# Performance work log

Measured on AMD Instinct MI355X. Metric: run time of the kernel, lower is better.

The kernel has to match this reference:

```python
import jax, jax.numpy as jnp
import numpy as np

B, N, D = 8, 1024, 1024
H = 16
HD = D // H  # 64
SCALE = float(HD) ** -0.5


def setup_inputs() -> dict:
    key = jax.random.key(0)
    k1, k2, k3 = jax.random.split(key, 3)
    x = jax.random.normal(k1, (B, N, D), dtype=jnp.float32)
    W_qkv = jax.random.normal(k2, (D, 3 * D), dtype=jnp.float32) * (D ** -0.5)
    b_qkv = jnp.zeros((3 * D,), dtype=jnp.float32)
    W_o = jax.random.normal(k3, (D, D), dtype=jnp.float32) * (D ** -0.5)
    b_o = jnp.zeros((D,), dtype=jnp.float32)
    return {"x": x, "W_qkv": W_qkv, "b_qkv": b_qkv, "W_o": W_o, "b_o": b_o}


def reference(x, W_qkv, b_qkv, W_o, b_o):
    b, n, _ = x.shape
    qkv = x @ W_qkv + b_qkv                      # (B, N, 3D)
    qkv = qkv.reshape(b, n, H, 3 * HD).transpose(0, 2, 1, 3)  # (B, H, N, 3*HD)
    q, k, v = jnp.split(qkv, 3, axis=-1)          # each (B, H, N, HD)
    attn = jnp.einsum('bhnd,bhmd->bhnm', q, k) * SCALE
    attn = jax.nn.softmax(attn, axis=-1)          # (B, H, N, N); dropout p=0 -> identity
    heads = jnp.einsum('bhnm,bhmd->bhnd', attn, v)
    heads = heads.transpose(0, 2, 1, 3).reshape(b, n, H * HD)  # (B, N, D)
    return heads @ W_o + b_o
```

## Files before the change

### kernel.cpp

```cpp
#include <hip/hip_runtime.h>
#include <hip/hip_bf16.h>

typedef unsigned short ushort_t;
typedef __bf16 bf16x8 __attribute__((ext_vector_type(8)));
typedef float floatx4 __attribute__((ext_vector_type(4)));

#define MFMA(a, b, c) __builtin_amdgcn_mfma_f32_16x16x32_bf16(a, b, c, 0, 0, 0)

__device__ __forceinline__ float b2f(ushort_t u) {
    union { ushort_t u; __hip_bfloat16 h; } cvt; cvt.u = u; return __bfloat162float(cvt.h);
}
__device__ __forceinline__ ushort_t f2b(float f) {
    union { ushort_t u; __hip_bfloat16 h; } cvt; cvt.h = __float2bfloat16(f); return cvt.u;
}

__device__ __forceinline__ void async_copy16(const ushort_t* g, ushort_t* l) {
    __builtin_amdgcn_global_load_lds(
        (const __attribute__((address_space(1))) void*)g,
        (__attribute__((address_space(3))) void*)l, 16, 0, 0);
}

__global__ void convert_x(const float* __restrict__ xin, ushort_t* __restrict__ xb) {
    int i = blockIdx.x * 256 + threadIdx.x;
    const float4* xf = (const float4*)xin;
    float4 a = xf[i * 2], b = xf[i * 2 + 1];
    union { ushort_t s[8]; uint4 v; } p;
    p.s[0] = f2b(a.x); p.s[1] = f2b(a.y); p.s[2] = f2b(a.z); p.s[3] = f2b(a.w);
    p.s[4] = f2b(b.x); p.s[5] = f2b(b.y); p.s[6] = f2b(b.z); p.s[7] = f2b(b.w);
    ((uint4*)xb)[i] = p.v;
}

__global__ void transpose_cvt(const float* __restrict__ W, ushort_t* __restrict__ Wt,
                              int K, int N) {
    __shared__ float tile[32][33];
    int n0 = blockIdx.x * 32, k0 = blockIdx.y * 32;
    int tx = threadIdx.x, ty = threadIdx.y;
#pragma unroll
    for (int i = 0; i < 4; ++i)
        tile[ty + i * 8][tx] = W[(size_t)(k0 + ty + i * 8) * N + n0 + tx];
    __syncthreads();
#pragma unroll
    for (int i = 0; i < 4; ++i)
        Wt[(size_t)(n0 + ty + i * 8) * K + k0 + tx] = f2b(tile[tx][ty + i * 8]);
}

__global__ __launch_bounds__(256, 3) void gemm_qkv(
    const ushort_t* __restrict__ A,
    const ushort_t* __restrict__ Bt,
    const float* __restrict__ bias,
    ushort_t* __restrict__ Qb, ushort_t* __restrict__ Kb, ushort_t* __restrict__ Vtb) {
    const int K = 1024;
    __shared__ __align__(16) ushort_t Alds[128 * 64];
    __shared__ __align__(16) ushort_t Blds[128 * 64];
    int tid = threadIdx.x;
    int wave = tid >> 6, lane = tid & 63;
    int quad = lane >> 4, l16 = lane & 15;
    int wm = (wave >> 1) * 64, wn = (wave & 1) * 64;
    int m0 = blockIdx.x * 128, n0 = blockIdx.y * 128;

    floatx4 acc[4][4] = {};

    int srow[4], scol[4];
#pragma unroll
    for (int p = 0; p < 4; ++p) {
        int slot = (wave * 4 + p) * 64 + lane;
        int row = slot >> 3;
        srow[p] = row;
        scol[p] = ((slot & 7) ^ (row & 7)) * 8;
    }

    for (int kt = 0; kt < 16; ++kt) {
        int k0 = kt * 64;
        __syncthreads();
#pragma unroll
        for (int p = 0; p < 4; ++p) {
            int t = wave * 4 + p;
            async_copy16(&A[(m0 + srow[p]) * K + k0 + scol[p]], &Alds[t * 512]);
            async_copy16(&Bt[(n0 + srow[p]) * K + k0 + scol[p]], &Blds[t * 512]);
        }
        __syncthreads();
#pragma unroll
        for (int ki = 0; ki < 2; ++ki) {
            bf16x8 af[4], bfv[4];
            int sc = ((ki * 4 + quad) ^ (l16 & 7)) * 8;
#pragma unroll
            for (int i = 0; i < 4; ++i) {
                __builtin_memcpy(&af[i],  &Alds[(wm + i * 16 + l16) * 64 + sc], 16);
                __builtin_memcpy(&bfv[i], &Blds[(wn + i * 16 + l16) * 64 + sc], 16);
            }
#pragma unroll
            for (int i = 0; i < 4; ++i)
#pragma unroll
                for (int j = 0; j < 4; ++j)
                    acc[i][j] = MFMA(af[i], bfv[j], acc[i][j]);
        }
    }

#pragma unroll
    for (int j = 0; j < 4; ++j) {
        int C = n0 + wn + j * 16 + l16;
        int h = C / 192;
        int r = C % 192;
        int which = r / 64;
        int d = r % 64;
        float bv = bias[C];
#pragma unroll
        for (int i = 0; i < 4; ++i) {
#pragma unroll
            for (int g = 0; g < 4; ++g) {
                int R = m0 + wm + i * 16 + quad * 4 + g;
                int b = R >> 10;
                int n_tok = R & 1023;
                ushort_t bits = f2b(acc[i][j][g] + bv);
                int bh = b * 16 + h;
                if (which == 0)      Qb[(bh * 1024 + n_tok) * 64 + d] = bits;
                else if (which == 1) Kb[(bh * 1024 + n_tok) * 64 + d] = bits;
                else                 Vtb[(bh * 64 + d) * 1024 + n_tok] = bits;
            }
        }
    }
}

__global__ __launch_bounds__(256, 3) void attn(
    const ushort_t* __restrict__ Qb, const ushort_t* __restrict__ Kb,
    const ushort_t* __restrict__ Vtb, ushort_t* __restrict__ heads) {
    __shared__ __align__(16) ushort_t Klds[64 * 64];
    __shared__ __align__(16) ushort_t Vlds[64 * 64];
    __shared__ __align__(16) ushort_t Plds[128 * 76];
    int tid = threadIdx.x;
    int wave = tid >> 6, lane = tid & 63;
    int quad = lane >> 4, l16 = lane & 15;
    int qt = blockIdx.x, h = blockIdx.y, b = blockIdx.z;
    int bh = b * 16 + h;
    const ushort_t* Qh = Qb + (size_t)bh * 65536;
    const ushort_t* Kh = Kb + (size_t)bh * 65536;
    const ushort_t* Vh = Vtb + (size_t)bh * 65536;

    bf16x8 qa[2][2];
#pragma unroll
    for (int mi = 0; mi < 2; ++mi) {
        int qrow = qt * 128 + wave * 32 + mi * 16 + l16;
        __builtin_memcpy(&qa[mi][0], &Qh[qrow * 64 + quad * 8], 16);
        __builtin_memcpy(&qa[mi][1], &Qh[qrow * 64 + 32 + quad * 8], 16);
    }

    floatx4 oacc[2][4] = {};
    floatx4 oext[2] = {};

    bf16x8 onesfrag;
    {
        ushort_t v = (l16 == 0) ? (ushort_t)0x3F80 : (ushort_t)0;
        ushort_t tmp[8] = {v, v, v, v, v, v, v, v};
        __builtin_memcpy(&onesfrag, tmp, 16);
    }

    const float C2 = 0.18033688f;

    int srow[2], scol[2];
#pragma unroll
    for (int p = 0; p < 2; ++p) {
        int slot = (wave * 2 + p) * 64 + lane;
        int row = slot >> 3;
        srow[p] = row;
        scol[p] = ((slot & 7) ^ (row & 7)) * 8;
    }

    for (int kt = 0; kt < 16; ++kt) {
        int key0 = kt * 64;
        __syncthreads();
#pragma unroll
        for (int p = 0; p < 2; ++p) {
            int t = wave * 2 + p;
            async_copy16(&Kh[(key0 + srow[p]) * 64 + scol[p]], &Klds[t * 512]);
            async_copy16(&Vh[srow[p] * 1024 + key0 + scol[p]], &Vlds[t * 512]);
        }
        __syncthreads();

#pragma unroll
        for (int mi = 0; mi < 2; ++mi) {
            floatx4 sacc[4];
#pragma unroll
            for (int n = 0; n < 4; ++n) {
                floatx4 z = {0.f, 0.f, 0.f, 0.f};
#pragma unroll
                for (int ki = 0; ki < 2; ++ki) {
                    bf16x8 bfv;
                    int sc = ((ki * 4 + quad) ^ (l16 & 7)) * 8;
                    __builtin_memcpy(&bfv, &Klds[(n * 16 + l16) * 64 + sc], 16);
                    z = MFMA(qa[mi][ki], bfv, z);
                }
                sacc[n] = z;
            }
#pragma unroll
            for (int n = 0; n < 4; ++n)
#pragma unroll
                for (int g = 0; g < 4; ++g) {
                    float arg = fminf(sacc[n][g] * C2, 50.f);
                    float pv = __builtin_exp2f(arg);
                    Plds[(wave * 32 + mi * 16 + quad * 4 + g) * 76 + n * 16 + l16] = f2b(pv);
                }
        }
        __syncthreads();

#pragma unroll
        for (int mi = 0; mi < 2; ++mi) {
            bf16x8 pa[2];
            int prow = wave * 32 + mi * 16 + l16;
#pragma unroll
            for (int ki = 0; ki < 2; ++ki)
                __builtin_memcpy(&pa[ki], &Plds[prow * 76 + ki * 32 + quad * 8], 16);
#pragma unroll
            for (int n = 0; n < 4; ++n)
#pragma unroll
                for (int ki = 0; ki < 2; ++ki) {
                    bf16x8 bfv;
                    int sc = ((ki * 4 + quad) ^ (l16 & 7)) * 8;
                    __builtin_memcpy(&bfv, &Vlds[(n * 16 + l16) * 64 + sc], 16);
                    oacc[mi][n] = MFMA(pa[ki], bfv, oacc[mi][n]);
                }
#pragma unroll
            for (int ki = 0; ki < 2; ++ki)
                oext[mi] = MFMA(pa[ki], onesfrag, oext[mi]);
        }
    }

#pragma unroll
    for (int mi = 0; mi < 2; ++mi)
#pragma unroll
        for (int g = 0; g < 4; ++g) {
            float l = __shfl(oext[mi][g], (lane & 48));
            float inv = 1.f / l;
            int n_tok = qt * 128 + wave * 32 + mi * 16 + quad * 4 + g;
#pragma unroll
            for (int n = 0; n < 4; ++n)
                heads[(size_t)(b * 1024 + n_tok) * 1024 + h * 64 + n * 16 + l16] =
                    f2b(oacc[mi][n][g] * inv);
        }
}

__global__ __launch_bounds__(256, 3) void gemm_out(
    const ushort_t* __restrict__ A,
    const ushort_t* __restrict__ Bt,
    const float* __restrict__ bias,
    float* __restrict__ out) {
    const int K = 1024;
    __shared__ __align__(16) ushort_t Alds[128 * 64];
    __shared__ __align__(16) ushort_t Blds[128 * 64];
    int tid = threadIdx.x;
    int wave = tid >> 6, lane = tid & 63;
    int quad = lane >> 4, l16 = lane & 15;
    int wm = (wave >> 1) * 64, wn = (wave & 1) * 64;
    int m0 = blockIdx.x * 128, n0 = blockIdx.y * 128;

    floatx4 acc[4][4] = {};

    int srow[4], scol[4];
#pragma unroll
    for (int p = 0; p < 4; ++p) {
        int slot = (wave * 4 + p) * 64 + lane;
        int row = slot >> 3;
        srow[p] = row;
        scol[p] = ((slot & 7) ^ (row & 7)) * 8;
    }

    for (int kt = 0; kt < 16; ++kt) {
        int k0 = kt * 64;
        __syncthreads();
#pragma unroll
        for (int p = 0; p < 4; ++p) {
            int t = wave * 4 + p;
            async_copy16(&A[(m0 + srow[p]) * K + k0 + scol[p]], &Alds[t * 512]);
            async_copy16(&Bt[(n0 + srow[p]) * K + k0 + scol[p]], &Blds[t * 512]);
        }
        __syncthreads();
#pragma unroll
        for (int ki = 0; ki < 2; ++ki) {
            bf16x8 af[4], bfv[4];
            int sc = ((ki * 4 + quad) ^ (l16 & 7)) * 8;
#pragma unroll
            for (int i = 0; i < 4; ++i) {
                __builtin_memcpy(&af[i],  &Alds[(wm + i * 16 + l16) * 64 + sc], 16);
                __builtin_memcpy(&bfv[i], &Blds[(wn + i * 16 + l16) * 64 + sc], 16);
            }
#pragma unroll
            for (int i = 0; i < 4; ++i)
#pragma unroll
                for (int j = 0; j < 4; ++j)
                    acc[i][j] = MFMA(af[i], bfv[j], acc[i][j]);
        }
    }

#pragma unroll
    for (int j = 0; j < 4; ++j) {
        int C = n0 + wn + j * 16 + l16;
        float bv = bias[C];
#pragma unroll
        for (int i = 0; i < 4; ++i)
#pragma unroll
            for (int g = 0; g < 4; ++g) {
                int R = m0 + wm + i * 16 + quad * 4 + g;
                out[(size_t)R * 1024 + C] = acc[i][j][g] + bv;
            }
    }
}

extern "C" void kernel_launch(void* const* d_in, const int* in_sizes, int n_in,
                              void* d_out, int out_size, void* d_ws, size_t ws_size,
                              hipStream_t stream) {
    const float* x    = (const float*)d_in[0];
    const float* Wqkv = (const float*)d_in[1];
    const float* bqkv = (const float*)d_in[2];
    const float* Wo   = (const float*)d_in[3];
    const float* bo   = (const float*)d_in[4];

    char* ws = (char*)d_ws;
    const size_t MB = 1u << 20;
    ushort_t* xb    = (ushort_t*)(ws);
    ushort_t* Qb    = (ushort_t*)(ws + 16 * MB);
    ushort_t* Kb    = (ushort_t*)(ws + 32 * MB);
    ushort_t* Vtb   = (ushort_t*)(ws + 48 * MB);
    ushort_t* heads = (ushort_t*)(ws + 64 * MB);
    ushort_t* WqkvT = (ushort_t*)(ws + 64 * MB);
    ushort_t* WoT   = (ushort_t*)(ws);

    convert_x<<<4096, 256, 0, stream>>>(x, xb);
    transpose_cvt<<<dim3(96, 32), dim3(32, 8), 0, stream>>>(Wqkv, WqkvT, 1024, 3072);
    gemm_qkv<<<dim3(64, 24), 256, 0, stream>>>(xb, WqkvT, bqkv, Qb, Kb, Vtb);
    attn<<<dim3(8, 16, 8), 256, 0, stream>>>(Qb, Kb, Vtb, heads);
    transpose_cvt<<<dim3(32, 32), dim3(32, 8), 0, stream>>>(Wo, WoT, 1024, 1024);
    gemm_out<<<dim3(64, 8), 256, 0, stream>>>(heads, WoT, bo, (float*)d_out);
}
```

Measured before the change: 265.8 us.

## Permute QKV weight columns so the GEMM epilogue writes coalesced Q/K/Vt

The QKV weight transpose now reorders output columns into [Q|K|V] blocks, so each GEMM tile maps to a single destination tensor. Q and K tiles store directly without per-element branching. V tiles are staged through a swizzled LDS buffer and written transposed as 16-byte vectors, replacing scattered 2-byte strided stores. In attention, K and V fragments are hoisted into registers once per tile, and S is computed as K·Q so P can be packed into 8-byte LDS stores; this costs more registers.

```diff
diff --git a/kernel.cpp b/kernel.cpp
--- a/kernel.cpp
+++ b/kernel.cpp
@@ -30,6 +30,21 @@
     ((uint4*)xb)[i] = p.v;
 }
 
+__global__ void transpose_cvt_qkv(const float* __restrict__ W, ushort_t* __restrict__ Wt) {
+    __shared__ float tile[32][33];
+    int p0 = blockIdx.x * 32, k0 = blockIdx.y * 32;
+    int which = p0 >> 10, rem = p0 & 1023;
+    int n0 = (rem >> 6) * 192 + which * 64 + (rem & 63);
+    int tx = threadIdx.x, ty = threadIdx.y;
+#pragma unroll
+    for (int i = 0; i < 4; ++i)
+        tile[ty + i * 8][tx] = W[(size_t)(k0 + ty + i * 8) * 3072 + n0 + tx];
+    __syncthreads();
+#pragma unroll
+    for (int i = 0; i < 4; ++i)
+        Wt[(size_t)(p0 + ty + i * 8) * 1024 + k0 + tx] = f2b(tile[tx][ty + i * 8]);
+}
+
 __global__ void transpose_cvt(const float* __restrict__ W, ushort_t* __restrict__ Wt,
                               int K, int N) {
     __shared__ float tile[32][33];
@@ -42,6 +57,10 @@
 #pragma unroll
     for (int i = 0; i < 4; ++i)
         Wt[(size_t)(n0 + ty + i * 8) * K + k0 + tx] = f2b(tile[tx][ty + i * 8]);
+}
+
+__device__ __forceinline__ int tswz(int n, int m) {
+    return n * 128 + (((m >> 3) ^ (n & 15)) << 3) + (m & 7);
 }
 
 __global__ __launch_bounds__(256, 3) void gemm_qkv(
@@ -50,8 +69,9 @@
     const float* __restrict__ bias,
     ushort_t* __restrict__ Qb, ushort_t* __restrict__ Kb, ushort_t* __restrict__ Vtb) {
     const int K = 1024;
-    __shared__ __align__(16) ushort_t Alds[128 * 64];
-    __shared__ __align__(16) ushort_t Blds[128 * 64];
+    __shared__ __align__(16) ushort_t SH[16384];
+    ushort_t* Alds = SH;
+    ushort_t* Blds = SH + 8192;
     int tid = threadIdx.x;
     int wave = tid >> 6, lane = tid & 63;
     int quad = lane >> 4, l16 = lane & 15;
@@ -96,27 +116,52 @@
         }
     }
 
-#pragma unroll
-    for (int j = 0; j < 4; ++j) {
-        int C = n0 + wn + j * 16 + l16;
-        int h = C / 192;
-        int r = C % 192;
-        int which = r / 64;
-        int d = r % 64;
-        float bv = bias[C];
-#pragma unroll
-        for (int i = 0; i < 4; ++i) {
-#pragma unroll
-            for (int g = 0; g < 4; ++g) {
-                int R = m0 + wm + i * 16 + quad * 4 + g;
-                int b = R >> 10;
-                int n_tok = R & 1023;
-                ushort_t bits = f2b(acc[i][j][g] + bv);
-                int bh = b * 16 + h;
-                if (which == 0)      Qb[(bh * 1024 + n_tok) * 64 + d] = bits;
-                else if (which == 1) Kb[(bh * 1024 + n_tok) * 64 + d] = bits;
-                else                 Vtb[(bh * 64 + d) * 1024 + n_tok] = bits;
-            }
+    int which = n0 >> 10;
+    int b = m0 >> 10;
+
+    if (which < 2) {
+        ushort_t* dst = which ? Kb : Qb;
+#pragma unroll
+        for (int j = 0; j < 4; ++j) {
+            int C = n0 + wn + j * 16 + l16;
+            int c = C & 1023;
+            int h = c >> 6, d = c & 63;
+            float bv = bias[((C >> 6) & 15) * 192 + which * 64 + (C & 63)];
+            size_t hb = (size_t)(b * 16 + h) * 65536 + d;
+#pragma unroll
+            for (int i = 0; i < 4; ++i)
+#pragma unroll
+                for (int g = 0; g < 4; ++g) {
+                    int n_tok = (m0 & 1023) + wm + i * 16 + quad * 4 + g;
+                    dst[hb + (size_t)n_tok * 64] = f2b(acc[i][j][g] + bv);
+                }
+        }
+    } else {
+        __syncthreads();
+#pragma unroll
+        for (int j = 0; j < 4; ++j) {
+            int C = n0 + wn + j * 16 + l16;
+            int nl = wn + j * 16 + l16;
+            float bv = bias[((C >> 6) & 15) * 192 + 128 + (C & 63)];
+#pragma unroll
+            for (int i = 0; i < 4; ++i)
+#pragma unroll
+                for (int g = 0; g < 4; ++g) {
+                    int ml = wm + i * 16 + quad * 4 + g;
+                    SH[tswz(nl, ml)] = f2b(acc[i][j][g] + bv);
+                }
+        }
+        __syncthreads();
+        int r = tid >> 1, half = tid & 1;
+        int vcol = (n0 - 2048) + r;
+        int h = vcol >> 6, d = vcol & 63;
+        size_t base = ((size_t)(b * 16 + h) * 64 + d) * 1024 + (m0 & 1023) + half * 64;
+#pragma unroll
+        for (int i8 = 0; i8 < 8; ++i8) {
+            int chunk = half * 8 + i8;
+            uint4 v;
+            __builtin_memcpy(&v, &SH[r * 128 + ((chunk ^ (r & 15)) << 3)], 16);
+            __builtin_memcpy(&Vtb[base + i8 * 8], &v, 16);
         }
     }
 }
@@ -176,32 +221,40 @@
         }
         __syncthreads();
 
+        bf16x8 kf[4][2];
+#pragma unroll
+        for (int n = 0; n < 4; ++n)
+#pragma unroll
+            for (int ki = 0; ki < 2; ++ki) {
+                int sc = ((ki * 4 + quad) ^ (l16 & 7)) * 8;
+                __builtin_memcpy(&kf[n][ki], &Klds[(n * 16 + l16) * 64 + sc], 16);
+            }
 #pragma unroll
         for (int mi = 0; mi < 2; ++mi) {
-            floatx4 sacc[4];
 #pragma unroll
             for (int n = 0; n < 4; ++n) {
                 floatx4 z = {0.f, 0.f, 0.f, 0.f};
 #pragma unroll
-                for (int ki = 0; ki < 2; ++ki) {
-                    bf16x8 bfv;
-                    int sc = ((ki * 4 + quad) ^ (l16 & 7)) * 8;
-                    __builtin_memcpy(&bfv, &Klds[(n * 16 + l16) * 64 + sc], 16);
-                    z = MFMA(qa[mi][ki], bfv, z);
-                }
-                sacc[n] = z;
-            }
-#pragma unroll
-            for (int n = 0; n < 4; ++n)
-#pragma unroll
-                for (int g = 0; g < 4; ++g) {
-                    float arg = fminf(sacc[n][g] * C2, 50.f);
-                    float pv = __builtin_exp2f(arg);
-                    Plds[(wave * 32 + mi * 16 + quad * 4 + g) * 76 + n * 16 + l16] = f2b(pv);
-                }
-        }
-        __syncthreads();
-
+                for (int ki = 0; ki < 2; ++ki)
+                    z = MFMA(kf[n][ki], qa[mi][ki], z);
+                union { ushort_t s[4]; double d8; } pk;
+#pragma unroll
+                for (int g = 0; g < 4; ++g)
+                    pk.s[g] = f2b(__builtin_exp2f(fminf(z[g] * C2, 50.f)));
+                __builtin_memcpy(
+                    &Plds[(wave * 32 + mi * 16 + l16) * 76 + n * 16 + quad * 4], &pk, 8);
+            }
+        }
+        __syncthreads();
+
+        bf16x8 vf[4][2];
+#pragma unroll
+        for (int n = 0; n < 4; ++n)
+#pragma unroll
+            for (int ki = 0; ki < 2; ++ki) {
+                int sc = ((ki * 4 + quad) ^ (l16 & 7)) * 8;
+                __builtin_memcpy(&vf[n][ki], &Vlds[(n * 16 + l16) * 64 + sc], 16);
+            }
 #pragma unroll
         for (int mi = 0; mi < 2; ++mi) {
             bf16x8 pa[2];
@@ -212,12 +265,8 @@
 #pragma unroll
             for (int n = 0; n < 4; ++n)
 #pragma unroll
-                for (int ki = 0; ki < 2; ++ki) {
-                    bf16x8 bfv;
-                    int sc = ((ki * 4 + quad) ^ (l16 & 7)) * 8;
-                    __builtin_memcpy(&bfv, &Vlds[(n * 16 + l16) * 64 + sc], 16);
-                    oacc[mi][n] = MFMA(pa[ki], bfv, oacc[mi][n]);
-                }
+                for (int ki = 0; ki < 2; ++ki)
+                    oacc[mi][n] = MFMA(pa[ki], vf[n][ki], oacc[mi][n]);
 #pragma unroll
             for (int ki = 0; ki < 2; ++ki)
                 oext[mi] = MFMA(pa[ki], onesfrag, oext[mi]);
@@ -324,7 +373,7 @@
     ushort_t* WoT   = (ushort_t*)(ws);
 
     convert_x<<<4096, 256, 0, stream>>>(x, xb);
-    transpose_cvt<<<dim3(96, 32), dim3(32, 8), 0, stream>>>(Wqkv, WqkvT, 1024, 3072);
+    transpose_cvt_qkv<<<dim3(96, 32), dim3(32, 8), 0, stream>>>(Wqkv, WqkvT);
     gemm_qkv<<<dim3(64, 24), 256, 0, stream>>>(xb, WqkvT, bqkv, Qb, Kb, Vtb);
     attn<<<dim3(8, 16, 8), 256, 0, stream>>>(Qb, Kb, Vtb, heads);
     transpose_cvt<<<dim3(32, 32), dim3(32, 8), 0, stream>>>(Wo, WoT, 1024, 1024);
```

Result: faster. 248.7 us (-6.4%).
